# Performance work log

Hardware: AMD Instinct MI355X
Metric: run time of the kernel (lower is better)

Reference implementation:

```python
import jax, jax.numpy as jnp
import numpy as np

N_NODES = 50000
N_EDGES = 400000
MUL0 = 16   # multiplicity of 0e irreps (scalars)
MUL1 = 8    # multiplicity of 1o irreps (vectors)
IN_DIM = MUL0 + 3 * MUL1          # 40
EDGE_FEAT = 32
W00 = MUL0 * MUL0                 # 0e x 0e -> 0e : 256
W10 = MUL1 * MUL1                 # 1o x 0e -> 1o : 64
W01 = MUL0 * MUL1                 # 0e x 1o -> 1o : 128
W11 = MUL1 * MUL0                 # 1o x 1o -> 0e : 128
WEIGHT_NUMEL = W00 + W10 + W01 + W11  # 576
INV_SQRT3 = 1.0 / np.sqrt(3.0).astype(np.float32)
# e3nn 'component' normalization with path_normalization='element':
# fan_in into each output irrep = sum over paths of mul1*mul2 = 16+8 = 24
ALPHA0 = np.float32(np.sqrt(1.0 / 24.0))  # sqrt((2*0+1)/fan_in)
ALPHA1 = np.float32(np.sqrt(3.0 / 24.0))  # sqrt((2*1+1)/fan_in)


def setup_inputs() -> dict:
    key = jax.random.key(0)
    ks = jax.random.split(key, 10)
    node_attr = jax.random.normal(ks[0], (N_NODES, IN_DIM), dtype=jnp.float32)
    edge_index = jax.random.randint(ks[1], (2, N_EDGES), 0, N_NODES, dtype=jnp.int32)
    edge_attr = jax.random.normal(ks[2], (N_EDGES, EDGE_FEAT), dtype=jnp.float32)
    edge_sh = jax.random.normal(ks[3], (N_EDGES, 4), dtype=jnp.float32)
    s = 1.0 / np.sqrt(EDGE_FEAT)
    w1 = jax.random.normal(ks[4], (EDGE_FEAT, EDGE_FEAT), dtype=jnp.float32) * s
    b1 = jnp.zeros((EDGE_FEAT,), dtype=jnp.float32)
    w2 = jax.random.normal(ks[5], (EDGE_FEAT, WEIGHT_NUMEL), dtype=jnp.float32) * s
    b2 = jnp.zeros((WEIGHT_NUMEL,), dtype=jnp.float32)
    return {"node_attr": node_attr, "edge_index": edge_index, "edge_attr": edge_attr,
            "edge_sh": edge_sh, "w1": w1, "b1": b1, "w2": w2, "b2": b2}


def _tp_conv(node_attr, edge_index, edge_attr, edge_sh, w1, b1, w2, b2):
    edge_src, edge_dst = edge_index[0], edge_index[1]
    # edge MLP -> per-edge tensor-product weights [E, 576]
    h = jax.nn.softplus(edge_attr @ w1 + b1)
    w = h @ w2 + b2
    w00 = w[:, :W00].reshape(-1, MUL0, MUL0)
    w10 = w[:, W00:W00 + W10].reshape(-1, MUL1, MUL1)
    w01 = w[:, W00 + W10:W00 + W10 + W01].reshape(-1, MUL0, MUL1)
    w11 = w[:, W00 + W10 + W01:].reshape(-1, MUL1, MUL0)
    # gather source features (node_attr[edge_dst]) and split irreps
    x = node_attr[edge_dst]                       # [E, 40]
    s0 = x[:, :MUL0]                              # [E, 16]  scalars 0e
    v1 = x[:, MUL0:].reshape(-1, MUL1, 3)         # [E, 8, 3] vectors 1o
    y0 = edge_sh[:, 0]                            # [E]      sh l=0
    y1 = edge_sh[:, 1:4]                          # [E, 3]   sh l=1
    # CG tensor product paths (unit-norm wigner 3j):
    # 0e x 0e -> 0e (w3j = 1) and 1o x 1o -> 0e (w3j = eps-free delta/sqrt3)
    out0 = ALPHA0 * (jnp.einsum('eu,e,euw->ew', s0, y0, w00)
                     + INV_SQRT3 * jnp.einsum('eum,em,euw->ew', v1, y1, w11))
    # 1o x 0e -> 1o and 0e x 1o -> 1o (w3j = delta/sqrt3)
    out1 = ALPHA1 * INV_SQRT3 * (jnp.einsum('eum,e,euw->ewm', v1, y0, w10)
                                 + jnp.einsum('eu,em,euw->ewm', s0, y1, w01))
    tp = jnp.concatenate([out0, out1.reshape(-1, 3 * MUL1)], axis=-1)  # [E, 40]
    # scatter-mean over edge_src
    n = node_attr.shape[0]
    summed = jax.ops.segment_sum(tp, edge_src, num_segments=n)
    counts = jax.ops.segment_sum(jnp.ones((tp.shape[0],), tp.dtype), edge_src, num_segments=n)
    out = summed / jnp.maximum(counts, 1.0)[:, None]
    # residual (out_dim == in_dim, so F.pad is a no-op)
    return out + node_attr


def reference(node_attr, edge_index, edge_attr, edge_sh, w1, b1, w2, b2):
    return _tp_conv(node_attr, edge_index, edge_attr, edge_sh, w1, b1, w2, b2)
```

## Files before the change

kernel.cpp:

```cpp
#include <hip/hip_runtime.h>
#include <hip/hip_bf16.h>
#include <math.h>

#define NNODES 50000
#define NEDGES 400000
#define ALPHA0f    0.20412414523193154f
#define INV_SQRT3f 0.57735026918962576f
#define TPROW      64

typedef short bf16x8 __attribute__((ext_vector_type(8)));
typedef float f32x4  __attribute__((ext_vector_type(4)));

__device__ __forceinline__ short f2bf(float x) {
    __hip_bfloat16 h = __float2bfloat16(x);
    return *reinterpret_cast<short*>(&h);
}
__device__ __forceinline__ float bf2f(unsigned short x) {
    return __uint_as_float(((unsigned)x) << 16);
}
__device__ __forceinline__ float softplus_f(float x) {
    return fmaxf(x, 0.0f) + __logf(1.0f + __expf(-fabsf(x)));
}

template<int MODE>
__global__ __launch_bounds__(512)
void tp_mfma_kernel(const float* __restrict__ node_attr,
                    const int*   __restrict__ edge_index,
                    const float* __restrict__ edge_attr,
                    const float* __restrict__ edge_sh,
                    const float* __restrict__ w1,
                    const float* __restrict__ b1,
                    const float* __restrict__ w2,
                    const float* __restrict__ b2,
                    unsigned short* __restrict__ tp_out,
                    int*   __restrict__ counts_i,
                    float* __restrict__ summed,
                    float* __restrict__ counts)
{
    __shared__ short w2f[36 * 512];
    __shared__ short w1f[2 * 512];
    __shared__ float b1s[32];
    __shared__ float b2s[576];
    __shared__ float xs[8][16][44];
    __shared__ short hs[8][16][48];
    __shared__ int   dsts[8][16];

    const int tid = threadIdx.x;

    for (int i = tid; i < 36 * 512; i += 512) {
        int col = i % 576, k = i / 576;
        int t = col >> 4, lr = col & 15, lg = k >> 3, j = k & 7;
        w2f[((t * 64 + (lr | (lg << 4))) * 8) + j] = f2bf(w2[i]);
    }
    for (int i = tid; i < 1024; i += 512) {
        int col = i & 31, k = i >> 5;
        int t = col >> 4, lr = col & 15, lg = k >> 3, j = k & 7;
        w1f[((t * 64 + (lr | (lg << 4))) * 8) + j] = f2bf(w1[i]);
    }
    if (tid < 32) b1s[tid] = b1[tid];
    for (int i = tid; i < 576; i += 512) b2s[i] = b2[i];
    __syncthreads();

    const int wid  = tid >> 6, lane = tid & 63;
    const int lrow = lane & 15, lgrp = lane >> 4;
    const int upar = lgrp >> 1;

    const bf16x8 w1a0 = *reinterpret_cast<const bf16x8*>(&w1f[lane * 8]);
    const bf16x8 w1a1 = *reinterpret_cast<const bf16x8*>(&w1f[512 + lane * 8]);
    const f32x4 b1c0 = *reinterpret_cast<const f32x4*>(&b1s[lgrp * 4]);
    const f32x4 b1c1 = *reinterpret_cast<const f32x4*>(&b1s[16 + lgrp * 4]);
    const f32x4 zero = {0.f, 0.f, 0.f, 0.f};

    bf16x8 b2a00, b2a01;
    #pragma unroll
    for (int j = 0; j < 8; ++j) {
        int u = lgrp * 8 + j;
        b2a00[j] = (u < 16) ? f2bf(b2[u * 16 + lrow]) : (short)0;
        b2a01[j] = (u < 16 && lrow < 8) ? f2bf(b2[320 + u * 8 + lrow]) : (short)0;
    }

    for (int g = blockIdx.x; g < NEDGES / 128; g += gridDim.x) {
        const int e0 = g * 128 + wid * 16;

        if (lane < 16) {
            int d = edge_index[NEDGES + e0 + lane];
            dsts[wid][lane] = d;
            float4 sh = *(const float4*)(edge_sh + (size_t)(e0 + lane) * 4);
            xs[wid][lane][40] = sh.x; xs[wid][lane][41] = sh.y;
            xs[wid][lane][42] = sh.z; xs[wid][lane][43] = sh.w;
        }
        #pragma unroll
        for (int it = 0; it < 3; ++it) {
            int idx = it * 64 + lane;
            if (idx < 160) {
                int ed = idx / 10, part = idx % 10;
                int d = dsts[wid][ed];
                float4 v = *(const float4*)(node_attr + (size_t)d * 40 + part * 4);
                *(float4*)&xs[wid][ed][part * 4] = v;
            }
        }

        const float4* ear = (const float4*)(edge_attr + (size_t)(e0 + lrow) * 32 + lgrp * 8);
        float4 ea0 = ear[0], ea1 = ear[1];
        bf16x8 bfrag;
        bfrag[0] = f2bf(ea0.x); bfrag[1] = f2bf(ea0.y); bfrag[2] = f2bf(ea0.z); bfrag[3] = f2bf(ea0.w);
        bfrag[4] = f2bf(ea1.x); bfrag[5] = f2bf(ea1.y); bfrag[6] = f2bf(ea1.z); bfrag[7] = f2bf(ea1.w);
        f32x4 c0 = __builtin_amdgcn_mfma_f32_16x16x32_bf16(w1a0, bfrag, b1c0, 0, 0, 0);
        f32x4 c1 = __builtin_amdgcn_mfma_f32_16x16x32_bf16(w1a1, bfrag, b1c1, 0, 0, 0);
        {
            short4 p0, p1;
            p0.x = f2bf(softplus_f(c0[0])); p0.y = f2bf(softplus_f(c0[1]));
            p0.z = f2bf(softplus_f(c0[2])); p0.w = f2bf(softplus_f(c0[3]));
            p1.x = f2bf(softplus_f(c1[0])); p1.y = f2bf(softplus_f(c1[1]));
            p1.z = f2bf(softplus_f(c1[2])); p1.w = f2bf(softplus_f(c1[3]));
            *(short4*)&hs[wid][lrow][lgrp * 4]      = p0;
            *(short4*)&hs[wid][lrow][16 + lgrp * 4] = p1;
        }
        const bf16x8 hfrag = *reinterpret_cast<const bf16x8*>(&hs[wid][lrow][lgrp * 8]);

        const float y0  = xs[wid][lrow][40];
        const float y1x = xs[wid][lrow][41];
        const float y1y = xs[wid][lrow][42];
        const float y1z = xs[wid][lrow][43];

        bf16x8 s0f;
        {
            f32x4 sA = *(const f32x4*)&xs[wid][lrow][(lgrp & 1) * 8];
            f32x4 sB = *(const f32x4*)&xs[wid][lrow][(lgrp & 1) * 8 + 4];
            bool live = (lgrp < 2);
            #pragma unroll
            for (int j = 0; j < 4; ++j) s0f[j]     = live ? f2bf(sA[j]) : (short)0;
            #pragma unroll
            for (int j = 0; j < 4; ++j) s0f[4 + j] = live ? f2bf(sB[j]) : (short)0;
        }
        f32x4 acc0 = __builtin_amdgcn_mfma_f32_16x16x32_bf16(b2a00, s0f, zero, 0, 0, 0);
        acc0 *= y0;
        f32x4 r01  = __builtin_amdgcn_mfma_f32_16x16x32_bf16(b2a01, s0f, zero, 0, 0, 0);
        f32x4 am0 = zero, am1 = zero, am2 = zero;

        #pragma unroll 1
        for (int t0 = 0; t0 < 16; t0 += 4) {
            f32x4 F4 = *(const f32x4*)&xs[wid][lrow][t0];
            #pragma unroll
            for (int q = 0; q < 4; ++q) {
                bf16x8 wa = *reinterpret_cast<const bf16x8*>(&w2f[((t0 + q) * 64 + lane) * 8]);
                f32x4 wv = __builtin_amdgcn_mfma_f32_16x16x32_bf16(wa, hfrag, zero, 0, 0, 0);
                acc0 += wv * (F4[q] * y0);
            }
        }
        #pragma unroll 4
        for (int tt = 0; tt < 4; ++tt) {
            int t = 16 + tt;
            bf16x8 wa = *reinterpret_cast<const bf16x8*>(&w2f[(t * 64 + lane) * 8]);
            f32x4 wv = __builtin_amdgcn_mfma_f32_16x16x32_bf16(wa, hfrag, zero, 0, 0, 0);
            f32x4 b2c = *reinterpret_cast<const f32x4*>(&b2s[t * 16 + lgrp * 4]);
            int u = 2 * tt + upar;
            f32x4 wb = wv + b2c;
            float f0 = y0 * xs[wid][lrow][16 + u * 3 + 0];
            float f1 = y0 * xs[wid][lrow][16 + u * 3 + 1];
            float f2 = y0 * xs[wid][lrow][16 + u * 3 + 2];
            am0 += wb * f0; am1 += wb * f1; am2 += wb * f2;
        }
        #pragma unroll 4
        for (int tt = 0; tt < 8; ++tt) {
            int t = 20 + tt;
            bf16x8 wa = *reinterpret_cast<const bf16x8*>(&w2f[(t * 64 + lane) * 8]);
            f32x4 wv = __builtin_amdgcn_mfma_f32_16x16x32_bf16(wa, hfrag, zero, 0, 0, 0);
            int u = 2 * tt + upar;
            float s = xs[wid][lrow][u];
            r01 += wv * s;
        }
        #pragma unroll 1
        for (int tt0 = 0; tt0 < 8; tt0 += 4) {
            f32x4 vA = *(const f32x4*)&xs[wid][lrow][16 + 3 * tt0];
            f32x4 vB = *(const f32x4*)&xs[wid][lrow][16 + 3 * tt0 + 4];
            f32x4 vC = *(const f32x4*)&xs[wid][lrow][16 + 3 * tt0 + 8];
            float e[12] = {vA[0], vA[1], vA[2], vA[3], vB[0], vB[1],
                           vB[2], vB[3], vC[0], vC[1], vC[2], vC[3]};
            #pragma unroll
            for (int q = 0; q < 4; ++q) {
                int t = 28 + tt0 + q;
                bf16x8 wa = *reinterpret_cast<const bf16x8*>(&w2f[(t * 64 + lane) * 8]);
                f32x4 wv = __builtin_amdgcn_mfma_f32_16x16x32_bf16(wa, hfrag, zero, 0, 0, 0);
                f32x4 b2c = *reinterpret_cast<const f32x4*>(&b2s[t * 16 + lgrp * 4]);
                float bu = INV_SQRT3f * (e[3 * q] * y1x + e[3 * q + 1] * y1y + e[3 * q + 2] * y1z);
                acc0 += (wv + b2c) * bu;
            }
        }

        #pragma unroll
        for (int r = 0; r < 4; ++r) {
            am0[r] += __shfl_xor(am0[r], 32);
            am1[r] += __shfl_xor(am1[r], 32);
            am2[r] += __shfl_xor(am2[r], 32);
            r01[r] += __shfl_xor(r01[r], 32);
        }

        if (MODE == 1) {
            #pragma unroll
            for (int r = 0; r < 4; ++r)
                xs[wid][lrow][lgrp * 4 + r] = ALPHA0f * acc0[r];
            if (lgrp < 2) {
                #pragma unroll
                for (int r = 0; r < 4; ++r) {
                    xs[wid][lrow][16 + lgrp * 12 + r * 3 + 0] = ALPHA0f * (am0[r] + y1x * r01[r]);
                    xs[wid][lrow][16 + lgrp * 12 + r * 3 + 1] = ALPHA0f * (am1[r] + y1y * r01[r]);
                    xs[wid][lrow][16 + lgrp * 12 + r * 3 + 2] = ALPHA0f * (am2[r] + y1z * r01[r]);
                }
            }
            #pragma unroll
            for (int it = 0; it < 3; ++it) {
                int idx = it * 64 + lane;
                if (idx < 160) {
                    int ed = idx / 10, part = idx % 10;
                    float4 v = *(float4*)&xs[wid][ed][part * 4];
                    short4 s;
                    s.x = f2bf(v.x); s.y = f2bf(v.y); s.z = f2bf(v.z); s.w = f2bf(v.w);
                    *(short4*)(tp_out + (size_t)(e0 + ed) * TPROW + part * 4) = s;
                }
            }
            if (lgrp == 0) atomicAdd(&counts_i[edge_index[e0 + lrow]], 1);
        } else {
            const int src = edge_index[e0 + lrow];
            float* row = summed + (size_t)src * 40;
            #pragma unroll
            for (int r = 0; r < 4; ++r)
                atomicAdd(row + lgrp * 4 + r, ALPHA0f * acc0[r]);
            if (lgrp < 2) {
                float* r1 = row + 16 + lgrp * 12;
                #pragma unroll
                for (int r = 0; r < 4; ++r) {
                    atomicAdd(r1 + r * 3 + 0, ALPHA0f * (am0[r] + y1x * r01[r]));
                    atomicAdd(r1 + r * 3 + 1, ALPHA0f * (am1[r] + y1y * r01[r]));
                    atomicAdd(r1 + r * 3 + 2, ALPHA0f * (am2[r] + y1z * r01[r]));
                }
            }
            if (lgrp == 0) atomicAdd(&counts[src], 1.0f);
        }
    }
}

extern "C" __global__ __launch_bounds__(256)
void scanA_kernel(const int* __restrict__ counts_i, int* __restrict__ offsets,
                  int* __restrict__ bsums)
{
    __shared__ int s[256];
    int t = threadIdx.x, id = blockIdx.x * 256 + t;
    int c = (id < NNODES) ? counts_i[id] : 0;
    s[t] = c; __syncthreads();
    #pragma unroll
    for (int off = 1; off < 256; off <<= 1) {
        int v = (t >= off) ? s[t - off] : 0;
        __syncthreads();
        s[t] += v;
        __syncthreads();
    }
    if (id < NNODES) offsets[id] = s[t] - c;
    if (t == 255) bsums[blockIdx.x] = s[255];
}

extern "C" __global__ __launch_bounds__(256)
void scanB_kernel(int* __restrict__ bsums, int nblocks)
{
    __shared__ int s[256];
    int t = threadIdx.x;
    int c = (t < nblocks) ? bsums[t] : 0;
    s[t] = c; __syncthreads();
    #pragma unroll
    for (int off = 1; off < 256; off <<= 1) {
        int v = (t >= off) ? s[t - off] : 0;
        __syncthreads();
        s[t] += v;
        __syncthreads();
    }
    if (t < nblocks) bsums[t] = s[t] - c;
}

extern "C" __global__ __launch_bounds__(256)
void scanC_kernel(int* __restrict__ offsets, const int* __restrict__ bsums,
                  int* __restrict__ cursor)
{
    int id = blockIdx.x * 256 + threadIdx.x;
    if (id < NNODES) {
        int o = offsets[id] + bsums[id >> 8];
        offsets[id] = o;
        cursor[id] = o;
    }
}

extern "C" __global__ __launch_bounds__(256)
void scatter_kernel(const int* __restrict__ edge_index, int* __restrict__ cursor,
                    int* __restrict__ csr)
{
    int e = blockIdx.x * 256 + threadIdx.x;
    if (e < NEDGES) {
        int src = edge_index[e];
        int pos = atomicAdd(&cursor[src], 1);
        csr[pos] = e;
    }
}

extern "C" __global__ __launch_bounds__(256)
void gather_kernel(const unsigned short* __restrict__ tp, const int* __restrict__ offsets,
                   const int* __restrict__ csr, const float* __restrict__ node_attr,
                   float* __restrict__ out)
{
    int gw = (blockIdx.x * 256 + threadIdx.x) >> 6;
    int lane = threadIdx.x & 63;
    int nwaves = (gridDim.x * 256) >> 6;
    for (int n = gw; n < NNODES; n += nwaves) {
        int start = offsets[n];
        int end = (n + 1 < NNODES) ? offsets[n + 1] : NEDGES;
        float a0 = 0.f, a1 = 0.f, a2 = 0.f, a3 = 0.f;
        int i = start;
        for (; i + 8 <= end; i += 8) {
            int i0 = csr[i],     i1 = csr[i + 1], i2 = csr[i + 2], i3 = csr[i + 3];
            int i4 = csr[i + 4], i5 = csr[i + 5], i6 = csr[i + 6], i7 = csr[i + 7];
            if (lane < 40) {
                a0 += bf2f(tp[(size_t)i0 * TPROW + lane]);
                a1 += bf2f(tp[(size_t)i1 * TPROW + lane]);
                a2 += bf2f(tp[(size_t)i2 * TPROW + lane]);
                a3 += bf2f(tp[(size_t)i3 * TPROW + lane]);
                a0 += bf2f(tp[(size_t)i4 * TPROW + lane]);
                a1 += bf2f(tp[(size_t)i5 * TPROW + lane]);
                a2 += bf2f(tp[(size_t)i6 * TPROW + lane]);
                a3 += bf2f(tp[(size_t)i7 * TPROW + lane]);
            }
        }
        for (; i + 2 <= end; i += 2) {
            int i0 = csr[i], i1 = csr[i + 1];
            if (lane < 40) {
                a0 += bf2f(tp[(size_t)i0 * TPROW + lane]);
                a1 += bf2f(tp[(size_t)i1 * TPROW + lane]);
            }
        }
        if (i < end) {
            int i0 = csr[i];
            if (lane < 40) a0 += bf2f(tp[(size_t)i0 * TPROW + lane]);
        }
        if (lane < 40) {
            float deg = (float)(end - start);
            out[(size_t)n * 40 + lane] =
                ((a0 + a1) + (a2 + a3)) / fmaxf(deg, 1.0f) + node_attr[(size_t)n * 40 + lane];
        }
    }
}

extern "C" __global__ __launch_bounds__(256)
void finalize_kernel(const float* __restrict__ summed,
                     const float* __restrict__ counts,
                     const float* __restrict__ node_attr,
                     float* __restrict__ out)
{
    int idx = blockIdx.x * 256 + threadIdx.x;
    if (idx < NNODES * 40) {
        int n = idx / 40;
        float c = fmaxf(counts[n], 1.0f);
        out[idx] = summed[idx] / c + node_attr[idx];
    }
}

extern "C" void kernel_launch(void* const* d_in, const int* in_sizes, int n_in,
                              void* d_out, int out_size, void* d_ws, size_t ws_size,
                              hipStream_t stream)
{
    const float* node_attr  = (const float*)d_in[0];
    const int*   edge_index = (const int*)  d_in[1];
    const float* edge_attr  = (const float*)d_in[2];
    const float* edge_sh    = (const float*)d_in[3];
    const float* w1 = (const float*)d_in[4];
    const float* b1 = (const float*)d_in[5];
    const float* w2 = (const float*)d_in[6];
    const float* b2 = (const float*)d_in[7];
    float* out = (float*)d_out;

    const int SCAN_BLOCKS = (NNODES + 255) / 256;
    const int EDGE_BLOCKS = (NEDGES + 255) / 256;
    const size_t NEED = (size_t)NEDGES * TPROW * 2 +
                        ((size_t)3 * NNODES + NEDGES + 256) * 4;

    if (ws_size >= NEED) {
        unsigned short* tp = (unsigned short*)d_ws;
        int* counts_i = (int*)(tp + (size_t)NEDGES * TPROW);
        int* offsets  = counts_i + NNODES;
        int* cursor   = offsets + NNODES;
        int* csr      = cursor + NNODES;
        int* bsums    = csr + NEDGES;

        hipMemsetAsync(counts_i, 0, (size_t)NNODES * 4, stream);

        hipLaunchKernelGGL((tp_mfma_kernel<1>), dim3(512), dim3(512), 0, stream,
                           node_attr, edge_index, edge_attr, edge_sh, w1, b1, w2, b2,
                           tp, counts_i, (float*)nullptr, (float*)nullptr);

        hipLaunchKernelGGL(scanA_kernel, dim3(SCAN_BLOCKS), dim3(256), 0, stream,
                           counts_i, offsets, bsums);
        hipLaunchKernelGGL(scanB_kernel, dim3(1), dim3(256), 0, stream,
                           bsums, SCAN_BLOCKS);
        hipLaunchKernelGGL(scanC_kernel, dim3(SCAN_BLOCKS), dim3(256), 0, stream,
                           offsets, bsums, cursor);
        hipLaunchKernelGGL(scatter_kernel, dim3(EDGE_BLOCKS), dim3(256), 0, stream,
                           edge_index, cursor, csr);
        hipLaunchKernelGGL(gather_kernel, dim3(2048), dim3(256), 0, stream,
                           tp, offsets, csr, node_attr, out);
    } else {
        float* summed = (float*)d_ws;
        float* counts = summed + (size_t)NNODES * 40;
        hipMemsetAsync(d_ws, 0, (size_t)(NNODES * 40 + NNODES) * sizeof(float), stream);
        hipLaunchKernelGGL((tp_mfma_kernel<0>), dim3(512), dim3(512), 0, stream,
                           node_attr, edge_index, edge_attr, edge_sh, w1, b1, w2, b2,
                           (unsigned short*)nullptr, (int*)nullptr, summed, counts);
        int fblk = (NNODES * 40 + 255) / 256;
        hipLaunchKernelGGL(finalize_kernel, dim3(fblk), dim3(256), 0, stream,
                           summed, counts, node_attr, out);
    }
}
```

Baseline: 131.9 us.

## Switch edge tensor-product kernel to 32x32x16 MFMA tiles with 32 edges per wave

The main edge kernel now has each wave process 32 edges using 32x32x16 bf16 MFMA instead of 16 edges with 16x16x32. The weight layout in LDS is reorganised to match. Gathered node features are staged in LDS as bf16, and the hidden activations are exchanged between half-waves through cross-lane shuffles instead of an LDS round trip. The aim is fewer MFMA issues per edge, less LDS traffic, and no cross-lane reduction at the end. In exchange the kernel needs more registers per lane and applies bf16 rounding to the node features earlier.

```diff
diff --git a/kernel.cpp b/kernel.cpp
--- a/kernel.cpp
+++ b/kernel.cpp
@@ -10,13 +10,22 @@
 
 typedef short bf16x8 __attribute__((ext_vector_type(8)));
 typedef float f32x4  __attribute__((ext_vector_type(4)));
+typedef float f32x16 __attribute__((ext_vector_type(16)));
+typedef unsigned int u32x4 __attribute__((ext_vector_type(4)));
 
 __device__ __forceinline__ short f2bf(float x) {
     __hip_bfloat16 h = __float2bfloat16(x);
     return *reinterpret_cast<short*>(&h);
 }
+__device__ __forceinline__ unsigned f2bfu(float x) {
+    __hip_bfloat16 h = __float2bfloat16(x);
+    return (unsigned)*reinterpret_cast<unsigned short*>(&h);
+}
 __device__ __forceinline__ float bf2f(unsigned short x) {
     return __uint_as_float(((unsigned)x) << 16);
+}
+__device__ __forceinline__ unsigned pack2(float a, float b) {
+    return f2bfu(a) | (f2bfu(b) << 16);
 }
 __device__ __forceinline__ float softplus_f(float x) {
     return fmaxf(x, 0.0f) + __logf(1.0f + __expf(-fabsf(x)));
@@ -37,205 +46,225 @@
                     float* __restrict__ summed,
                     float* __restrict__ counts)
 {
-    __shared__ short w2f[36 * 512];
-    __shared__ short w1f[2 * 512];
+    __shared__ short w2f[18 * 2 * 512];
     __shared__ float b1s[32];
     __shared__ float b2s[576];
-    __shared__ float xs[8][16][44];
-    __shared__ short hs[8][16][48];
-    __shared__ int   dsts[8][16];
+    __shared__ unsigned short xsb[8][32][44];
 
     const int tid = threadIdx.x;
 
-    for (int i = tid; i < 36 * 512; i += 512) {
+    for (int i = tid; i < 18432; i += 512) {
         int col = i % 576, k = i / 576;
-        int t = col >> 4, lr = col & 15, lg = k >> 3, j = k & 7;
-        w2f[((t * 64 + (lr | (lg << 4))) * 8) + j] = f2bf(w2[i]);
-    }
-    for (int i = tid; i < 1024; i += 512) {
-        int col = i & 31, k = i >> 5;
-        int t = col >> 4, lr = col & 15, lg = k >> 3, j = k & 7;
-        w1f[((t * 64 + (lr | (lg << 4))) * 8) + j] = f2bf(w1[i]);
+        int t = col >> 5, lr = col & 31, kh = k >> 4, lg = (k >> 3) & 1, j = k & 7;
+        w2f[(((t * 2 + kh) * 64) + (lr | (lg << 5))) * 8 + j] = f2bf(w2[i]);
     }
     if (tid < 32) b1s[tid] = b1[tid];
     for (int i = tid; i < 576; i += 512) b2s[i] = b2[i];
     __syncthreads();
 
-    const int wid  = tid >> 6, lane = tid & 63;
-    const int lrow = lane & 15, lgrp = lane >> 4;
-    const int upar = lgrp >> 1;
-
-    const bf16x8 w1a0 = *reinterpret_cast<const bf16x8*>(&w1f[lane * 8]);
-    const bf16x8 w1a1 = *reinterpret_cast<const bf16x8*>(&w1f[512 + lane * 8]);
-    const f32x4 b1c0 = *reinterpret_cast<const f32x4*>(&b1s[lgrp * 4]);
-    const f32x4 b1c1 = *reinterpret_cast<const f32x4*>(&b1s[16 + lgrp * 4]);
-    const f32x4 zero = {0.f, 0.f, 0.f, 0.f};
-
-    bf16x8 b2a00, b2a01;
+    const int wid = tid >> 6, lane = tid & 63;
+    const int le = lane & 31, s = lane >> 5;
+
+    bf16x8 w1a0, w1a1;
     #pragma unroll
     for (int j = 0; j < 8; ++j) {
-        int u = lgrp * 8 + j;
-        b2a00[j] = (u < 16) ? f2bf(b2[u * 16 + lrow]) : (short)0;
-        b2a01[j] = (u < 16 && lrow < 8) ? f2bf(b2[320 + u * 8 + lrow]) : (short)0;
-    }
-
-    for (int g = blockIdx.x; g < NEDGES / 128; g += gridDim.x) {
-        const int e0 = g * 128 + wid * 16;
-
-        if (lane < 16) {
-            int d = edge_index[NEDGES + e0 + lane];
-            dsts[wid][lane] = d;
-            float4 sh = *(const float4*)(edge_sh + (size_t)(e0 + lane) * 4);
-            xs[wid][lane][40] = sh.x; xs[wid][lane][41] = sh.y;
-            xs[wid][lane][42] = sh.z; xs[wid][lane][43] = sh.w;
-        }
+        w1a0[j] = f2bf(w1[(s * 8 + j) * 32 + le]);
+        w1a1[j] = f2bf(w1[(16 + s * 8 + j) * 32 + le]);
+    }
+    bf16x8 ab;
+    #pragma unroll
+    for (int j = 0; j < 8; ++j) {
+        int u = s * 8 + j;
+        float v = (le < 16) ? b2[u * 16 + le]
+                : (le < 24) ? b2[320 + u * 8 + (le - 16)] : 0.0f;
+        ab[j] = f2bf(v);
+    }
+    f32x16 zero16;
+    #pragma unroll
+    for (int i = 0; i < 16; ++i) zero16[i] = 0.0f;
+
+    const int NGROUPS = (NEDGES + 255) / 256;
+
+    for (int g = blockIdx.x; g < NGROUPS; g += gridDim.x) {
+        const int e0 = g * 256 + wid * 32;
+        if (e0 >= NEDGES) continue;
+
+        int dval = (lane < 32) ? edge_index[NEDGES + e0 + lane] : 0;
         #pragma unroll
-        for (int it = 0; it < 3; ++it) {
-            int idx = it * 64 + lane;
-            if (idx < 160) {
-                int ed = idx / 10, part = idx % 10;
-                int d = dsts[wid][ed];
-                float4 v = *(const float4*)(node_attr + (size_t)d * 40 + part * 4);
-                *(float4*)&xs[wid][ed][part * 4] = v;
-            }
-        }
-
-        const float4* ear = (const float4*)(edge_attr + (size_t)(e0 + lrow) * 32 + lgrp * 8);
-        float4 ea0 = ear[0], ea1 = ear[1];
-        bf16x8 bfrag;
-        bfrag[0] = f2bf(ea0.x); bfrag[1] = f2bf(ea0.y); bfrag[2] = f2bf(ea0.z); bfrag[3] = f2bf(ea0.w);
-        bfrag[4] = f2bf(ea1.x); bfrag[5] = f2bf(ea1.y); bfrag[6] = f2bf(ea1.z); bfrag[7] = f2bf(ea1.w);
-        f32x4 c0 = __builtin_amdgcn_mfma_f32_16x16x32_bf16(w1a0, bfrag, b1c0, 0, 0, 0);
-        f32x4 c1 = __builtin_amdgcn_mfma_f32_16x16x32_bf16(w1a1, bfrag, b1c1, 0, 0, 0);
+        for (int it = 0; it < 5; ++it) {
+            int c = it * 64 + lane;
+            int row = c / 10, part = c % 10;
+            int d = __shfl(dval, row);
+            float4 v = *(const float4*)(node_attr + (size_t)d * 40 + part * 4);
+            short4 sx;
+            sx.x = f2bf(v.x); sx.y = f2bf(v.y); sx.z = f2bf(v.z); sx.w = f2bf(v.w);
+            *(short4*)&xsb[wid][row][part * 4] = sx;
+        }
+        const float4 sh = *(const float4*)(edge_sh + (size_t)(e0 + le) * 4);
+        const float y0 = sh.x, y1x = sh.y, y1y = sh.z, y1z = sh.w;
+        const int srcv = edge_index[e0 + le];
+
+        const float* ear = edge_attr + (size_t)(e0 + le) * 32;
+        bf16x8 bf1a, bf1b;
         {
-            short4 p0, p1;
-            p0.x = f2bf(softplus_f(c0[0])); p0.y = f2bf(softplus_f(c0[1]));
-            p0.z = f2bf(softplus_f(c0[2])); p0.w = f2bf(softplus_f(c0[3]));
-            p1.x = f2bf(softplus_f(c1[0])); p1.y = f2bf(softplus_f(c1[1]));
-            p1.z = f2bf(softplus_f(c1[2])); p1.w = f2bf(softplus_f(c1[3]));
-            *(short4*)&hs[wid][lrow][lgrp * 4]      = p0;
-            *(short4*)&hs[wid][lrow][16 + lgrp * 4] = p1;
-        }
-        const bf16x8 hfrag = *reinterpret_cast<const bf16x8*>(&hs[wid][lrow][lgrp * 8]);
-
-        const float y0  = xs[wid][lrow][40];
-        const float y1x = xs[wid][lrow][41];
-        const float y1y = xs[wid][lrow][42];
-        const float y1z = xs[wid][lrow][43];
+            float4 a0 = *(const float4*)(ear + s * 8);
+            float4 a1 = *(const float4*)(ear + s * 8 + 4);
+            float4 b0 = *(const float4*)(ear + 16 + s * 8);
+            float4 b1v = *(const float4*)(ear + 16 + s * 8 + 4);
+            bf1a[0]=f2bf(a0.x); bf1a[1]=f2bf(a0.y); bf1a[2]=f2bf(a0.z); bf1a[3]=f2bf(a0.w);
+            bf1a[4]=f2bf(a1.x); bf1a[5]=f2bf(a1.y); bf1a[6]=f2bf(a1.z); bf1a[7]=f2bf(a1.w);
+            bf1b[0]=f2bf(b0.x); bf1b[1]=f2bf(b0.y); bf1b[2]=f2bf(b0.z); bf1b[3]=f2bf(b0.w);
+            bf1b[4]=f2bf(b1v.x); bf1b[5]=f2bf(b1v.y); bf1b[6]=f2bf(b1v.z); bf1b[7]=f2bf(b1v.w);
+        }
+        f32x16 c1 = __builtin_amdgcn_mfma_f32_32x32x16_bf16(w1a0, bf1a, zero16, 0, 0, 0);
+        c1 = __builtin_amdgcn_mfma_f32_32x32x16_bf16(w1a1, bf1b, c1, 0, 0, 0);
+
+        unsigned P[8];
+        #pragma unroll
+        for (int q = 0; q < 8; ++q) {
+            int r0 = 2 * q, r1 = 2 * q + 1;
+            int j0 = (r0 & 3) + 8 * (r0 >> 2) + 4 * s;
+            int j1 = (r1 & 3) + 8 * (r1 >> 2) + 4 * s;
+            P[q] = pack2(softplus_f(c1[r0] + b1s[j0]), softplus_f(c1[r1] + b1s[j1]));
+        }
+        unsigned x0 = (unsigned)__shfl_xor((int)(s ? P[0] : P[2]), 32);
+        unsigned x1 = (unsigned)__shfl_xor((int)(s ? P[1] : P[3]), 32);
+        unsigned x2 = (unsigned)__shfl_xor((int)(s ? P[4] : P[6]), 32);
+        unsigned x3 = (unsigned)__shfl_xor((int)(s ? P[5] : P[7]), 32);
+        u32x4 hw0, hw1;
+        hw0[0] = s ? x0 : P[0];  hw0[1] = s ? x1 : P[1];
+        hw0[2] = s ? P[2] : x0;  hw0[3] = s ? P[3] : x1;
+        hw1[0] = s ? x2 : P[4];  hw1[1] = s ? x3 : P[5];
+        hw1[2] = s ? P[6] : x2;  hw1[3] = s ? P[7] : x3;
+        const bf16x8 hf0 = *reinterpret_cast<bf16x8*>(&hw0);
+        const bf16x8 hf1 = *reinterpret_cast<bf16x8*>(&hw1);
 
         bf16x8 s0f;
         {
-            f32x4 sA = *(const f32x4*)&xs[wid][lrow][(lgrp & 1) * 8];
-            f32x4 sB = *(const f32x4*)&xs[wid][lrow][(lgrp & 1) * 8 + 4];
-            bool live = (lgrp < 2);
-            #pragma unroll
-            for (int j = 0; j < 4; ++j) s0f[j]     = live ? f2bf(sA[j]) : (short)0;
-            #pragma unroll
-            for (int j = 0; j < 4; ++j) s0f[4 + j] = live ? f2bf(sB[j]) : (short)0;
-        }
-        f32x4 acc0 = __builtin_amdgcn_mfma_f32_16x16x32_bf16(b2a00, s0f, zero, 0, 0, 0);
-        acc0 *= y0;
-        f32x4 r01  = __builtin_amdgcn_mfma_f32_16x16x32_bf16(b2a01, s0f, zero, 0, 0, 0);
-        f32x4 am0 = zero, am1 = zero, am2 = zero;
-
+            short4 a = *(const short4*)&xsb[wid][le][s * 8];
+            short4 b = *(const short4*)&xsb[wid][le][s * 8 + 4];
+            s0f[0]=a.x; s0f[1]=a.y; s0f[2]=a.z; s0f[3]=a.w;
+            s0f[4]=b.x; s0f[5]=b.y; s0f[6]=b.z; s0f[7]=b.w;
+        }
+        f32x16 dbias = __builtin_amdgcn_mfma_f32_32x32x16_bf16(ab, s0f, zero16, 0, 0, 0);
+
+        float acc0[8], r01[4], am0[4], am1[4], am2[4];
+        #pragma unroll
+        for (int i = 0; i < 8; ++i) acc0[i] = dbias[i] * y0;
+        #pragma unroll
+        for (int i = 0; i < 4; ++i) { r01[i] = dbias[8 + i];
+                                      am0[i] = 0.f; am1[i] = 0.f; am2[i] = 0.f; }
+
+        #pragma unroll 2
+        for (int t = 0; t < 8; ++t) {
+            bf16x8 wa0 = *reinterpret_cast<const bf16x8*>(&w2f[((t * 2 + 0) * 64 + lane) * 8]);
+            bf16x8 wa1 = *reinterpret_cast<const bf16x8*>(&w2f[((t * 2 + 1) * 64 + lane) * 8]);
+            f32x16 wv = __builtin_amdgcn_mfma_f32_32x32x16_bf16(wa0, hf0, zero16, 0, 0, 0);
+            wv = __builtin_amdgcn_mfma_f32_32x32x16_bf16(wa1, hf1, wv, 0, 0, 0);
+            float F0 = bf2f(xsb[wid][le][2 * t])     * y0;
+            float F1 = bf2f(xsb[wid][le][2 * t + 1]) * y0;
+            #pragma unroll
+            for (int r = 0; r < 8; ++r) acc0[r] += wv[r] * F0;
+            #pragma unroll
+            for (int r = 0; r < 8; ++r) acc0[r] += wv[8 + r] * F1;
+        }
         #pragma unroll 1
-        for (int t0 = 0; t0 < 16; t0 += 4) {
-            f32x4 F4 = *(const f32x4*)&xs[wid][lrow][t0];
+        for (int tt = 0; tt < 2; ++tt) {
+            int tb = (8 + tt) * 2;
+            bf16x8 wa0 = *reinterpret_cast<const bf16x8*>(&w2f[((tb + 0) * 64 + lane) * 8]);
+            bf16x8 wa1 = *reinterpret_cast<const bf16x8*>(&w2f[((tb + 1) * 64 + lane) * 8]);
+            f32x16 wv = __builtin_amdgcn_mfma_f32_32x32x16_bf16(wa0, hf0, zero16, 0, 0, 0);
+            wv = __builtin_amdgcn_mfma_f32_32x32x16_bf16(wa1, hf1, wv, 0, 0, 0);
             #pragma unroll
             for (int q = 0; q < 4; ++q) {
-                bf16x8 wa = *reinterpret_cast<const bf16x8*>(&w2f[((t0 + q) * 64 + lane) * 8]);
-                f32x4 wv = __builtin_amdgcn_mfma_f32_16x16x32_bf16(wa, hfrag, zero, 0, 0, 0);
-                acc0 += wv * (F4[q] * y0);
-            }
-        }
-        #pragma unroll 4
+                int u = 4 * tt + q;
+                float f0 = y0 * bf2f(xsb[wid][le][16 + u * 3 + 0]);
+                float f1 = y0 * bf2f(xsb[wid][le][16 + u * 3 + 1]);
+                float f2 = y0 * bf2f(xsb[wid][le][16 + u * 3 + 2]);
+                f32x4 b2q = *(const f32x4*)&b2s[256 + tt * 32 + 8 * q + 4 * s];
+                #pragma unroll
+                for (int k = 0; k < 4; ++k) {
+                    float wb = wv[4 * q + k] + b2q[k];
+                    am0[k] += wb * f0; am1[k] += wb * f1; am2[k] += wb * f2;
+                }
+            }
+        }
+        #pragma unroll 1
         for (int tt = 0; tt < 4; ++tt) {
-            int t = 16 + tt;
-            bf16x8 wa = *reinterpret_cast<const bf16x8*>(&w2f[(t * 64 + lane) * 8]);
-            f32x4 wv = __builtin_amdgcn_mfma_f32_16x16x32_bf16(wa, hfrag, zero, 0, 0, 0);
-            f32x4 b2c = *reinterpret_cast<const f32x4*>(&b2s[t * 16 + lgrp * 4]);
-            int u = 2 * tt + upar;
-            f32x4 wb = wv + b2c;
-            float f0 = y0 * xs[wid][lrow][16 + u * 3 + 0];
-            float f1 = y0 * xs[wid][lrow][16 + u * 3 + 1];
-            float f2 = y0 * xs[wid][lrow][16 + u * 3 + 2];
-            am0 += wb * f0; am1 += wb * f1; am2 += wb * f2;
-        }
-        #pragma unroll 4
-        for (int tt = 0; tt < 8; ++tt) {
-            int t = 20 + tt;
-            bf16x8 wa = *reinterpret_cast<const bf16x8*>(&w2f[(t * 64 + lane) * 8]);
-            f32x4 wv = __builtin_amdgcn_mfma_f32_16x16x32_bf16(wa, hfrag, zero, 0, 0, 0);
-            int u = 2 * tt + upar;
-            float s = xs[wid][lrow][u];
-            r01 += wv * s;
+            int tb = (10 + tt) * 2;
+            bf16x8 wa0 = *reinterpret_cast<const bf16x8*>(&w2f[((tb + 0) * 64 + lane) * 8]);
+            bf16x8 wa1 = *reinterpret_cast<const bf16x8*>(&w2f[((tb + 1) * 64 + lane) * 8]);
+            f32x16 wv = __builtin_amdgcn_mfma_f32_32x32x16_bf16(wa0, hf0, zero16, 0, 0, 0);
+            wv = __builtin_amdgcn_mfma_f32_32x32x16_bf16(wa1, hf1, wv, 0, 0, 0);
+            #pragma unroll
+            for (int q = 0; q < 4; ++q) {
+                float su = bf2f(xsb[wid][le][4 * tt + q]);
+                #pragma unroll
+                for (int k = 0; k < 4; ++k) r01[k] += wv[4 * q + k] * su;
+            }
         }
         #pragma unroll 1
-        for (int tt0 = 0; tt0 < 8; tt0 += 4) {
-            f32x4 vA = *(const f32x4*)&xs[wid][lrow][16 + 3 * tt0];
-            f32x4 vB = *(const f32x4*)&xs[wid][lrow][16 + 3 * tt0 + 4];
-            f32x4 vC = *(const f32x4*)&xs[wid][lrow][16 + 3 * tt0 + 8];
-            float e[12] = {vA[0], vA[1], vA[2], vA[3], vB[0], vB[1],
-                           vB[2], vB[3], vC[0], vC[1], vC[2], vC[3]};
-            #pragma unroll
-            for (int q = 0; q < 4; ++q) {
-                int t = 28 + tt0 + q;
-                bf16x8 wa = *reinterpret_cast<const bf16x8*>(&w2f[(t * 64 + lane) * 8]);
-                f32x4 wv = __builtin_amdgcn_mfma_f32_16x16x32_bf16(wa, hfrag, zero, 0, 0, 0);
-                f32x4 b2c = *reinterpret_cast<const f32x4*>(&b2s[t * 16 + lgrp * 4]);
-                float bu = INV_SQRT3f * (e[3 * q] * y1x + e[3 * q + 1] * y1y + e[3 * q + 2] * y1z);
-                acc0 += (wv + b2c) * bu;
-            }
-        }
-
+        for (int tt = 0; tt < 4; ++tt) {
+            int tb = (14 + tt) * 2;
+            bf16x8 wa0 = *reinterpret_cast<const bf16x8*>(&w2f[((tb + 0) * 64 + lane) * 8]);
+            bf16x8 wa1 = *reinterpret_cast<const bf16x8*>(&w2f[((tb + 1) * 64 + lane) * 8]);
+            f32x16 wv = __builtin_amdgcn_mfma_f32_32x32x16_bf16(wa0, hf0, zero16, 0, 0, 0);
+            wv = __builtin_amdgcn_mfma_f32_32x32x16_bf16(wa1, hf1, wv, 0, 0, 0);
+            int u0 = 2 * tt, u1 = 2 * tt + 1;
+            float bu0 = INV_SQRT3f * (bf2f(xsb[wid][le][16 + u0 * 3 + 0]) * y1x +
+                                      bf2f(xsb[wid][le][16 + u0 * 3 + 1]) * y1y +
+                                      bf2f(xsb[wid][le][16 + u0 * 3 + 2]) * y1z);
+            float bu1 = INV_SQRT3f * (bf2f(xsb[wid][le][16 + u1 * 3 + 0]) * y1x +
+                                      bf2f(xsb[wid][le][16 + u1 * 3 + 1]) * y1y +
+                                      bf2f(xsb[wid][le][16 + u1 * 3 + 2]) * y1z);
+            f32x4 bq0 = *(const f32x4*)&b2s[448 + tt * 32 + 4 * s];
+            f32x4 bq1 = *(const f32x4*)&b2s[448 + tt * 32 + 8 + 4 * s];
+            f32x4 bq2 = *(const f32x4*)&b2s[448 + tt * 32 + 16 + 4 * s];
+            f32x4 bq3 = *(const f32x4*)&b2s[448 + tt * 32 + 24 + 4 * s];
+            #pragma unroll
+            for (int k = 0; k < 4; ++k) {
+                acc0[k]     += (wv[k]      + bq0[k]) * bu0;
+                acc0[4 + k] += (wv[4 + k]  + bq1[k]) * bu0;
+                acc0[k]     += (wv[8 + k]  + bq2[k]) * bu1;
+                acc0[4 + k] += (wv[12 + k] + bq3[k]) * bu1;
+            }
+        }
+
+        float o1[12];
         #pragma unroll
-        for (int r = 0; r < 4; ++r) {
-            am0[r] += __shfl_xor(am0[r], 32);
-            am1[r] += __shfl_xor(am1[r], 32);
-            am2[r] += __shfl_xor(am2[r], 32);
-            r01[r] += __shfl_xor(r01[r], 32);
-        }
-
+        for (int w = 0; w < 4; ++w) {
+            o1[w * 3 + 0] = ALPHA0f * (am0[w] + y1x * r01[w]);
+            o1[w * 3 + 1] = ALPHA0f * (am1[w] + y1y * r01[w]);
+            o1[w * 3 + 2] = ALPHA0f * (am2[w] + y1z * r01[w]);
+        }
         if (MODE == 1) {
-            #pragma unroll
-            for (int r = 0; r < 4; ++r)
-                xs[wid][lrow][lgrp * 4 + r] = ALPHA0f * acc0[r];
-            if (lgrp < 2) {
-                #pragma unroll
-                for (int r = 0; r < 4; ++r) {
-                    xs[wid][lrow][16 + lgrp * 12 + r * 3 + 0] = ALPHA0f * (am0[r] + y1x * r01[r]);
-                    xs[wid][lrow][16 + lgrp * 12 + r * 3 + 1] = ALPHA0f * (am1[r] + y1y * r01[r]);
-                    xs[wid][lrow][16 + lgrp * 12 + r * 3 + 2] = ALPHA0f * (am2[r] + y1z * r01[r]);
-                }
-            }
-            #pragma unroll
-            for (int it = 0; it < 3; ++it) {
-                int idx = it * 64 + lane;
-                if (idx < 160) {
-                    int ed = idx / 10, part = idx % 10;
-                    float4 v = *(float4*)&xs[wid][ed][part * 4];
-                    short4 s;
-                    s.x = f2bf(v.x); s.y = f2bf(v.y); s.z = f2bf(v.z); s.w = f2bf(v.w);
-                    *(short4*)(tp_out + (size_t)(e0 + ed) * TPROW + part * 4) = s;
-                }
-            }
-            if (lgrp == 0) atomicAdd(&counts_i[edge_index[e0 + lrow]], 1);
+            unsigned short* rowp = tp_out + (size_t)(e0 + le) * TPROW;
+            short4 sa, sb;
+            sa.x = f2bf(ALPHA0f * acc0[0]); sa.y = f2bf(ALPHA0f * acc0[1]);
+            sa.z = f2bf(ALPHA0f * acc0[2]); sa.w = f2bf(ALPHA0f * acc0[3]);
+            sb.x = f2bf(ALPHA0f * acc0[4]); sb.y = f2bf(ALPHA0f * acc0[5]);
+            sb.z = f2bf(ALPHA0f * acc0[6]); sb.w = f2bf(ALPHA0f * acc0[7]);
+            *(short4*)(rowp + 4 * s)     = sa;
+            *(short4*)(rowp + 8 + 4 * s) = sb;
+            #pragma unroll
+            for (int q = 0; q < 3; ++q) {
+                short4 sq;
+                sq.x = f2bf(o1[q * 4 + 0]); sq.y = f2bf(o1[q * 4 + 1]);
+                sq.z = f2bf(o1[q * 4 + 2]); sq.w = f2bf(o1[q * 4 + 3]);
+                *(short4*)(rowp + 16 + 12 * s + q * 4) = sq;
+            }
+            if (s == 0) atomicAdd(&counts_i[srcv], 1);
         } else {
-            const int src = edge_index[e0 + lrow];
-            float* row = summed + (size_t)src * 40;
-            #pragma unroll
-            for (int r = 0; r < 4; ++r)
-                atomicAdd(row + lgrp * 4 + r, ALPHA0f * acc0[r]);
-            if (lgrp < 2) {
-                float* r1 = row + 16 + lgrp * 12;
-                #pragma unroll
-                for (int r = 0; r < 4; ++r) {
-                    atomicAdd(r1 + r * 3 + 0, ALPHA0f * (am0[r] + y1x * r01[r]));
-                    atomicAdd(r1 + r * 3 + 1, ALPHA0f * (am1[r] + y1y * r01[r]));
-                    atomicAdd(r1 + r * 3 + 2, ALPHA0f * (am2[r] + y1z * r01[r]));
-                }
-            }
-            if (lgrp == 0) atomicAdd(&counts[src], 1.0f);
+            float* row = summed + (size_t)srcv * 40;
+            #pragma unroll
+            for (int i = 0; i < 4; ++i) {
+                atomicAdd(row + i + 4 * s,     ALPHA0f * acc0[i]);
+                atomicAdd(row + 8 + i + 4 * s, ALPHA0f * acc0[4 + i]);
+            }
+            #pragma unroll
+            for (int q = 0; q < 12; ++q)
+                atomicAdd(row + 16 + 12 * s + q, o1[q]);
+            if (s == 0) atomicAdd(&counts[srcv], 1.0f);
         }
     }
 }
@@ -244,36 +273,36 @@
 void scanA_kernel(const int* __restrict__ counts_i, int* __restrict__ offsets,
                   int* __restrict__ bsums)
 {
-    __shared__ int s[256];
+    __shared__ int sm[256];
     int t = threadIdx.x, id = blockIdx.x * 256 + t;
     int c = (id < NNODES) ? counts_i[id] : 0;
-    s[t] = c; __syncthreads();
+    sm[t] = c; __syncthreads();
     #pragma unroll
     for (int off = 1; off < 256; off <<= 1) {
-        int v = (t >= off) ? s[t - off] : 0;
+        int v = (t >= off) ? sm[t - off] : 0;
         __syncthreads();
-        s[t] += v;
+        sm[t] += v;
         __syncthreads();
     }
-    if (id < NNODES) offsets[id] = s[t] - c;
-    if (t == 255) bsums[blockIdx.x] = s[255];
+    if (id < NNODES) offsets[id] = sm[t] - c;
+    if (t == 255) bsums[blockIdx.x] = sm[255];
 }
 
 extern "C" __global__ __launch_bounds__(256)
 void scanB_kernel(int* __restrict__ bsums, int nblocks)
 {
-    __shared__ int s[256];
+    __shared__ int sm[256];
     int t = threadIdx.x;
     int c = (t < nblocks) ? bsums[t] : 0;
-    s[t] = c; __syncthreads();
+    sm[t] = c; __syncthreads();
     #pragma unroll
     for (int off = 1; off < 256; off <<= 1) {
-        int v = (t >= off) ? s[t - off] : 0;
+        int v = (t >= off) ? sm[t - off] : 0;
         __syncthreads();
-        s[t] += v;
+        sm[t] += v;
         __syncthreads();
     }
-    if (t < nblocks) bsums[t] = s[t] - c;
+    if (t < nblocks) bsums[t] = sm[t] - c;
 }
 
 extern "C" __global__ __launch_bounds__(256)
```

New measurement: 117.8 us (median of 3 runs). 10.7% less time.
